# Kernel optimization log

Measured on AMD Instinct MI355X. Metric: run time of the kernel, lower is better.

Reference implementation:

```python
import jax, jax.numpy as jnp
import numpy as np

KQ_DIM = 132  # latent_dim == kq_dim so gather covers full rows
EPS = 1e-12


def setup_inputs() -> dict:
    key = jax.random.key(0)
    ks = jax.random.split(key, 8)
    B, C, H, W = 8, 3, 128, 128
    N, K, D = 2048, 32, KQ_DIM
    indices = jax.random.randint(ks[0], (3, B, N, K), 0, H * W + 1, dtype=jnp.int32)
    img = jax.random.normal(ks[1], (B, C, H, W), dtype=jnp.float32)
    # stand-in backbone: 3x3 conv (ResidualDenseNetwork not in source)
    conv_w = jax.random.normal(ks[2], (D, C, 3, 3), dtype=jnp.float32) * (1.0 / np.sqrt(C * 9))
    conv_b = jnp.zeros((D,), dtype=jnp.float32)
    sc = 1.0 / np.sqrt(D)
    ks_w = jax.random.normal(ks[3], (D, D), dtype=jnp.float32) * sc
    ks_b = jax.random.normal(ks[4], (D,), dtype=jnp.float32) * sc
    qs_w = jax.random.normal(ks[5], (D, D), dtype=jnp.float32) * sc
    qs_b = jax.random.normal(ks[6], (D,), dtype=jnp.float32) * sc
    return {"indices": indices, "img": img, "conv_w": conv_w, "conv_b": conv_b,
            "ks_w": ks_w, "ks_b": ks_b, "qs_w": qs_w, "qs_b": qs_b}


def reference(indices, img, conv_w, conv_b, ks_w, ks_b, qs_w, qs_b):
    _, B, N, K = indices.shape
    # backbone conv: [B, D, H, W]
    feat = jax.lax.conv_general_dilated(
        img, conv_w, window_strides=(1, 1), padding='SAME',
        dimension_numbers=('NCHW', 'OIHW', 'NCHW')) + conv_b[None, :, None, None]
    # torch F.normalize(dim=-1) BEFORE permute -> L2 over last spatial (width) axis
    norm = jnp.linalg.norm(feat, axis=-1, keepdims=True)
    feat = feat / jnp.maximum(norm, EPS)
    # permute(0,2,3,1): [B, H, W, D] -> flatten spatial
    feat = jnp.transpose(feat, (0, 2, 3, 1))
    Bf, Hh, Ww, D = feat.shape
    flat = feat.reshape(Bf, Hh * Ww, D)
    flat = jnp.concatenate([flat, jnp.zeros((Bf, 1, D), dtype=flat.dtype)], axis=1)
    flat_ks = flat @ ks_w.T + ks_b  # [B, WH+1, D]
    flat_qs = flat @ qs_w.T + qs_b
    x_idx = indices[1].reshape(B, N * K)  # [B, N*K]
    y_idx = indices[2].reshape(B, N * K)
    x_feat = jnp.take_along_axis(flat_ks, x_idx[:, :, None], axis=1).reshape(B, N, K, D)
    y_feat = jnp.take_along_axis(flat_qs, y_idx[:, :, None], axis=1).reshape(B, N, K, D)
    # entailment logits: scaled dot product over feature dim
    logits = (x_feat * y_feat).sum(axis=-1) * (D ** -0.5)  # [B, N, K]
    return logits
```

## Files before the change

kernel.cpp:

```cpp
#include <hip/hip_runtime.h>
#include <hip/hip_bf16.h>
#include <math.h>

#define B_ 8
#define H_ 128
#define W_ 128
#define C_ 3
#define D_ 132
#define HW_ (H_*W_)
#define RPB_ (HW_+1)
#define NROWS_ (B_*RPB_)
#define AROWS_ 131136
#define FSTRIDE_ 136
#define MSTRIDE_ 168
#define NK_ 65536
#define NOUT_ (B_*NK_)
#define MELEMS_ 24576

typedef __attribute__((ext_vector_type(8))) short short8v;
typedef __attribute__((ext_vector_type(8))) unsigned short ushort8v;
typedef __attribute__((ext_vector_type(4))) float f32x4;

#define GLOAD16(gp, lp) __builtin_amdgcn_global_load_lds( \
  (const __attribute__((address_space(1))) unsigned int*)(gp), \
  (__attribute__((address_space(3))) unsigned int*)(void*)(lp), 16, 0, 0)

__device__ inline float bf2f(unsigned short u) {
  return __uint_as_float(((unsigned)u) << 16);
}
__device__ inline unsigned short f2bf(float f) {
  __hip_bfloat16 hb = __float2bfloat16(f);
  return *(unsigned short*)&hb;
}

__global__ __launch_bounds__(512, 4) void fused_prep_conv_kernel(
    const float* __restrict__ img, const float* __restrict__ cw,
    const float* __restrict__ cb, unsigned short* __restrict__ flat,
    const float* __restrict__ ks_w, const float* __restrict__ ks_b,
    const float* __restrict__ qs_w, const float* __restrict__ qs_b,
    unsigned short* __restrict__ Mb, float* __restrict__ cc) {
  int bid = blockIdx.x;
  int tid = threadIdx.x;

  if (bid > B_ * H_) {
    int idx = (bid - (B_ * H_ + 1)) * 512 + tid;
    if (idx >= MELEMS_) return;
    int a = idx / MSTRIDE_;
    int k = idx - a * MSTRIDE_;
    float val = 0.f;
    if (k < D_) {
      if (a < D_) {
        for (int o = 0; o < D_; ++o)
          val = fmaf(ks_w[o * D_ + a], qs_w[o * D_ + k], val);
      } else if (a == 132) {
        for (int o = 0; o < D_; ++o)
          val = fmaf(qs_b[o], ks_w[o * D_ + k], val);
      } else if (a == 133) {
        for (int o = 0; o < D_; ++o)
          val = fmaf(ks_b[o], qs_w[o * D_ + k], val);
      }
    }
    Mb[idx] = f2bf(val);
    if (idx == 0) {
      float s = 0.f;
      for (int o = 0; o < D_; ++o) s = fmaf(ks_b[o], qs_b[o], s);
      cc[0] = s;
    }
    return;
  }
  if (bid == B_ * H_) {
    for (int i = tid; i < B_ * FSTRIDE_; i += 512) {
      int b = i / FSTRIDE_, d = i - (i / FSTRIDE_) * FSTRIDE_;
      flat[((size_t)b * RPB_ + HW_) * FSTRIDE_ + d] = (d == 132) ? 0x3F80 : 0;
    }
    return;
  }
  int b = bid >> 7, h = bid & 127;

  __shared__ __align__(16) float in_s[9][132];
  __shared__ float w_s[D_ * 27];
  __shared__ float b_s[D_];
  __shared__ float parts[8][132];
  __shared__ float nscale[132];

  for (int i = tid; i < 9 * 132; i += 512) {
    int ck = i / 132, x = i - ck * 132;
    int c = ck / 3, kh = ck - c * 3;
    int hh = h + kh - 1, ww = x - 1;
    float val = 0.f;
    if (x >= 1 && x <= 128 && hh >= 0 && hh < H_)
      val = img[((size_t)(b * C_ + c) * H_ + hh) * W_ + ww];
    in_s[ck][x] = val;
  }
  for (int i = tid; i < D_ * 27; i += 512) w_s[i] = cw[i];
  if (tid < D_) b_s[tid] = cb[tid];
  __syncthreads();

  auto conv16 = [&](int item, float* acc) {
    int wg = item / 132;
    int d = item - wg * 132;
    float wt[27];
#pragma unroll
    for (int j = 0; j < 27; ++j) wt[j] = w_s[d * 27 + j];
    float bias = b_s[d];
#pragma unroll
    for (int i = 0; i < 16; ++i) acc[i] = bias;
    int q = wg * 4;
#pragma unroll
    for (int ck = 0; ck < 9; ++ck) {
      const float4* p4 = (const float4*)&in_s[ck][0];
      float v[20];
#pragma unroll
      for (int j = 0; j < 5; ++j) {
        float4 t4 = p4[q + j];
        v[4 * j + 0] = t4.x; v[4 * j + 1] = t4.y;
        v[4 * j + 2] = t4.z; v[4 * j + 3] = t4.w;
      }
#pragma unroll
      for (int i = 0; i < 16; ++i) {
        float a0 = fmaf(v[i], wt[ck * 3 + 0], acc[i]);
        float a1 = fmaf(v[i + 1], wt[ck * 3 + 1], a0);
        acc[i] = fmaf(v[i + 2], wt[ck * 3 + 2], a1);
      }
    }
    float ssq = 0.f;
#pragma unroll
    for (int i = 0; i < 16; ++i) ssq = fmaf(acc[i], acc[i], ssq);
    parts[wg][d] = ssq;
  };

  float acc0[16], acc1[16], acc2[16];
  conv16(tid, acc0);
  conv16(tid + 512, acc1);
  if (tid < 32) conv16(tid + 1024, acc2);
  __syncthreads();

  if (tid < 132) {
    float s = 0.f;
#pragma unroll
    for (int wg = 0; wg < 8; ++wg) s += parts[wg][tid];
    nscale[tid] = 1.f / fmaxf(sqrtf(s), 1e-12f);
  }
  __syncthreads();

  size_t rowbase = (size_t)b * RPB_ + (size_t)h * W_;
  auto store16 = [&](int item, const float* acc) {
    int wg = item / 132;
    int d = item - wg * 132;
    float sc = nscale[d];
#pragma unroll
    for (int i = 0; i < 16; ++i)
      flat[(rowbase + wg * 16 + i) * FSTRIDE_ + d] = f2bf(acc[i] * sc);
  };
  store16(tid, acc0);
  store16(tid + 512, acc1);
  if (tid < 32) store16(tid + 1024, acc2);

  if (tid < 128) {
    uint2 tailv; tailv.x = 0x3F80u; tailv.y = 0u;
    *(uint2*)&flat[(rowbase + tid) * FSTRIDE_ + 132] = tailv;
  }
}

__global__ __launch_bounds__(256, 2) void gemm_kernel(
    unsigned short* __restrict__ fb, const unsigned short* __restrict__ Mb,
    const float* __restrict__ cc, unsigned short* __restrict__ zb) {
  __shared__ __align__(16) unsigned short As[64 * FSTRIDE_ + 64];
  __shared__ __align__(16) unsigned short Ms[MELEMS_];
  int tid = threadIdx.x, wave = tid >> 6, lane = tid & 63;
  size_t row0 = (size_t)blockIdx.x * 64;

  for (int ch = wave; ch < 48; ch += 4)
    GLOAD16(Mb + (size_t)ch * 512 + lane * 8, Ms + ch * 512);
  const unsigned short* Ag = fb + row0 * FSTRIDE_;
  for (int ch = wave; ch < 17; ch += 4)
    GLOAD16(Ag + (size_t)ch * 512 + lane * 8, As + ch * 512);
  if (tid < 64) As[64 * FSTRIDE_ + tid] = 0;
  __syncthreads();

  int c15 = lane & 15, kg = lane >> 4;
  const unsigned short* arow = &As[(wave * 16 + c15) * FSTRIDE_ + kg * 8];
  const unsigned short* brow = &Ms[c15 * MSTRIDE_ + kg * 8];
  f32x4 acc[9] = {};
#pragma unroll
  for (int ks = 0; ks < 5; ++ks) {
    short8v af = *(const short8v*)(arow + ks * 32);
#pragma unroll
    for (int ct = 0; ct < 9; ++ct) {
      short8v bf = *(const short8v*)(brow + ct * 16 * MSTRIDE_ + ks * 32);
      acc[ct] = __builtin_amdgcn_mfma_f32_16x16x32_bf16(af, bf, acc[ct], 0, 0, 0);
    }
  }

  float cval = cc[0];
  size_t rbase = row0 + wave * 16 + kg * 4;
#pragma unroll
  for (int ct = 0; ct < 9; ++ct) {
    int col = ct * 16 + c15;
#pragma unroll
    for (int j = 0; j < 4; ++j) {
      size_t r = rbase + j;
      if (r < NROWS_) {
        if (col < D_)            zb[r * FSTRIDE_ + col] = f2bf(acc[ct][j]);
        else if (col == 132)     fb[r * FSTRIDE_ + 133] = f2bf(acc[ct][j]);
        else if (col == 133)     zb[r * FSTRIDE_ + 132] = f2bf(acc[ct][j] + cval);
        else if (col == 134)     zb[r * FSTRIDE_ + 133] = 0x3F80;
        else if (col == 135)     zb[r * FSTRIDE_ + 134] = 0;
        else if (col == 136)     zb[r * FSTRIDE_ + 135] = 0;
      }
    }
  }
}

__global__ __launch_bounds__(256) void gather_kernel(
    const int* __restrict__ xi, const int* __restrict__ yi,
    const unsigned short* __restrict__ flat, const unsigned short* __restrict__ zb,
    float* __restrict__ out) {
  const float scale = 0.08703882797784892f;
  int bi = blockIdx.x;
  int b = bi & 7;
  int chunk = bi >> 3;
  int rem = chunk * 32 + (threadIdx.x >> 3);
  int lane = threadIdx.x & 7;
  size_t ib = (size_t)b * NK_ + rem;
  int x = xi[ib], y = yi[ib];
  const unsigned short* fx = flat + ((size_t)b * RPB_ + x) * FSTRIDE_;
  const unsigned short* zy = zb + ((size_t)b * RPB_ + y) * FSTRIDE_;
  float acc = 0.f;
#pragma unroll
  for (int leg = 0; leg < 2; ++leg) {
    int e0 = leg * 64 + lane * 8;
    ushort8v a8 = *(const ushort8v*)(fx + e0);
    ushort8v z8 = *(const ushort8v*)(zy + e0);
#pragma unroll
    for (int t = 0; t < 8; ++t)
      acc = fmaf(bf2f(a8[t]), bf2f(z8[t]), acc);
  }
  if (lane == 0) {
    ushort8v a8 = *(const ushort8v*)(fx + 128);
    ushort8v z8 = *(const ushort8v*)(zy + 128);
#pragma unroll
    for (int t = 0; t < 8; ++t)
      acc = fmaf(bf2f(a8[t]), bf2f(z8[t]), acc);
  }
  acc += __shfl_xor(acc, 1);
  acc += __shfl_xor(acc, 2);
  acc += __shfl_xor(acc, 4);
  if (lane == 0)
    out[((size_t)b << 16) | rem] = acc * scale;
}

extern "C" void kernel_launch(void* const* d_in, const int* in_sizes, int n_in,
                              void* d_out, int out_size, void* d_ws, size_t ws_size,
                              hipStream_t stream) {
  const int* indices  = (const int*)d_in[0];
  const float* img    = (const float*)d_in[1];
  const float* conv_w = (const float*)d_in[2];
  const float* conv_b = (const float*)d_in[3];
  const float* ks_w   = (const float*)d_in[4];
  const float* ks_b   = (const float*)d_in[5];
  const float* qs_w   = (const float*)d_in[6];
  const float* qs_b   = (const float*)d_in[7];
  float* out = (float*)d_out;

  char* w = (char*)d_ws;
  unsigned short* flatb = (unsigned short*)w;
  size_t off = (size_t)AROWS_ * FSTRIDE_ * 2;
  unsigned short* zbuf = (unsigned short*)(w + off); off += (size_t)AROWS_ * FSTRIDE_ * 2;
  unsigned short* Mb = (unsigned short*)(w + off);   off += MELEMS_ * 2;
  float* cc = (float*)(w + off);

  const int* xi = indices + (size_t)B_ * NK_;
  const int* yi = indices + (size_t)2 * B_ * NK_;

  hipLaunchKernelGGL(fused_prep_conv_kernel, dim3(B_ * H_ + 1 + MELEMS_ / 512),
                     dim3(512), 0, stream,
                     img, conv_w, conv_b, flatb, ks_w, ks_b, qs_w, qs_b, Mb, cc);
  hipLaunchKernelGGL(gemm_kernel, dim3(AROWS_ / 64), dim3(256), 0, stream,
                     flatb, Mb, cc, zbuf);
  hipLaunchKernelGGL(gather_kernel, dim3(NOUT_ / 32), dim3(256), 0, stream,
                     xi, yi, flatb, zbuf, out);
}
```

Before: 92.35 us.

## Fuse conv/normalize with bilinear GEMM per image row; split weight prep kernel

```diff
diff --git a/kernel.cpp b/kernel.cpp
--- a/kernel.cpp
+++ b/kernel.cpp
@@ -12,10 +12,11 @@
 #define NROWS_ (B_*RPB_)
 #define AROWS_ 131136
 #define FSTRIDE_ 136
-#define MSTRIDE_ 168
+#define MSTRIDE_ 160
+#define MROWS_ 144
+#define MELEMS_ (MROWS_*MSTRIDE_)
 #define NK_ 65536
 #define NOUT_ (B_*NK_)
-#define MELEMS_ 24576
 
 typedef __attribute__((ext_vector_type(8))) short short8v;
 typedef __attribute__((ext_vector_type(8))) unsigned short ushort8v;
@@ -33,56 +34,102 @@
   return *(unsigned short*)&hb;
 }
 
-__global__ __launch_bounds__(512, 4) void fused_prep_conv_kernel(
-    const float* __restrict__ img, const float* __restrict__ cw,
-    const float* __restrict__ cb, unsigned short* __restrict__ flat,
+__global__ __launch_bounds__(512) void prep_kernel(
     const float* __restrict__ ks_w, const float* __restrict__ ks_b,
     const float* __restrict__ qs_w, const float* __restrict__ qs_b,
     unsigned short* __restrict__ Mb, float* __restrict__ cc) {
+  int idx = blockIdx.x * 512 + threadIdx.x;
+  if (idx >= MELEMS_) return;
+  int a = idx / MSTRIDE_;
+  int k = idx - a * MSTRIDE_;
+  float val = 0.f;
+  if (k < D_) {
+    if (a < D_) {
+      for (int o = 0; o < D_; ++o)
+        val = fmaf(ks_w[o * D_ + a], qs_w[o * D_ + k], val);
+    } else if (a == 132) {
+      for (int o = 0; o < D_; ++o)
+        val = fmaf(qs_b[o], ks_w[o * D_ + k], val);
+    } else if (a == 133) {
+      for (int o = 0; o < D_; ++o)
+        val = fmaf(ks_b[o], qs_w[o * D_ + k], val);
+    }
+  }
+  Mb[idx] = f2bf(val);
+  if (idx == 0) {
+    float s = 0.f;
+    for (int o = 0; o < D_; ++o) s = fmaf(ks_b[o], qs_b[o], s);
+    cc[0] = s;
+  }
+}
+
+__device__ __forceinline__ float conv_item16(
+    const float* __restrict__ in_s, const float* __restrict__ w_s,
+    float bias, int d, int w0, float* acc) {
+  float wt[27];
+#pragma unroll
+  for (int j = 0; j < 27; ++j) wt[j] = w_s[d * 27 + j];
+#pragma unroll
+  for (int i = 0; i < 16; ++i) acc[i] = bias;
+#pragma unroll
+  for (int ck = 0; ck < 9; ++ck) {
+    const float4* p4 = (const float4*)(in_s + ck * 132);
+    float v[20];
+#pragma unroll
+    for (int j = 0; j < 5; ++j) {
+      float4 t4 = p4[(w0 >> 2) + j];
+      v[4 * j + 0] = t4.x; v[4 * j + 1] = t4.y;
+      v[4 * j + 2] = t4.z; v[4 * j + 3] = t4.w;
+    }
+#pragma unroll
+    for (int i = 0; i < 16; ++i) {
+      float a0 = fmaf(v[i], wt[ck * 3 + 0], acc[i]);
+      float a1 = fmaf(v[i + 1], wt[ck * 3 + 1], a0);
+      acc[i] = fmaf(v[i + 2], wt[ck * 3 + 2], a1);
+    }
+  }
+  float ssq = 0.f;
+#pragma unroll
+  for (int i = 0; i < 16; ++i) ssq = fmaf(acc[i], acc[i], ssq);
+  return ssq;
+}
+
+__global__ __launch_bounds__(512, 4) void fused_conv_gemm_kernel(
+    const float* __restrict__ img, const float* __restrict__ cw,
+    const float* __restrict__ cb, unsigned short* __restrict__ fb,
+    const unsigned short* __restrict__ Mb, const float* __restrict__ cc,
+    unsigned short* __restrict__ zb) {
   int bid = blockIdx.x;
   int tid = threadIdx.x;
 
-  if (bid > B_ * H_) {
-    int idx = (bid - (B_ * H_ + 1)) * 512 + tid;
-    if (idx >= MELEMS_) return;
-    int a = idx / MSTRIDE_;
-    int k = idx - a * MSTRIDE_;
-    float val = 0.f;
-    if (k < D_) {
-      if (a < D_) {
-        for (int o = 0; o < D_; ++o)
-          val = fmaf(ks_w[o * D_ + a], qs_w[o * D_ + k], val);
-      } else if (a == 132) {
-        for (int o = 0; o < D_; ++o)
-          val = fmaf(qs_b[o], ks_w[o * D_ + k], val);
-      } else if (a == 133) {
-        for (int o = 0; o < D_; ++o)
-          val = fmaf(ks_b[o], qs_w[o * D_ + k], val);
-      }
-    }
-    Mb[idx] = f2bf(val);
-    if (idx == 0) {
-      float s = 0.f;
-      for (int o = 0; o < D_; ++o) s = fmaf(ks_b[o], qs_b[o], s);
-      cc[0] = s;
-    }
-    return;
-  }
   if (bid == B_ * H_) {
+    float cval = cc[0];
     for (int i = tid; i < B_ * FSTRIDE_; i += 512) {
       int b = i / FSTRIDE_, d = i - (i / FSTRIDE_) * FSTRIDE_;
-      flat[((size_t)b * RPB_ + HW_) * FSTRIDE_ + d] = (d == 132) ? 0x3F80 : 0;
+      size_t r = (size_t)b * RPB_ + HW_;
+      fb[r * FSTRIDE_ + d] = (d == 132) ? 0x3F80 : 0;
+      unsigned short zv = 0;
+      if (d == 132) zv = f2bf(cval);
+      else if (d == 133) zv = 0x3F80;
+      zb[r * FSTRIDE_ + d] = zv;
     }
     return;
   }
+
+  int wave = tid >> 6, lane = tid & 63;
+  __shared__ __align__(16) unsigned short Ms[MELEMS_];
+  __shared__ float nscale[132];
+  __shared__ __align__(16) char un[34880];
+  float* in_s = (float*)un;
+  float* w_s  = in_s + 9 * 132;
+  float* b_s  = w_s + 132 * 27;
+  float* parts = b_s + 132;
+  unsigned short* As = (unsigned short*)un;
+
+  for (int ch = wave; ch < 45; ch += 8)
+    GLOAD16(Mb + (size_t)ch * 512 + lane * 8, Ms + ch * 512);
+
   int b = bid >> 7, h = bid & 127;
-
-  __shared__ __align__(16) float in_s[9][132];
-  __shared__ float w_s[D_ * 27];
-  __shared__ float b_s[D_];
-  __shared__ float parts[8][132];
-  __shared__ float nscale[132];
-
   for (int i = tid; i < 9 * 132; i += 512) {
     int ck = i / 132, x = i - ck * 132;
     int c = ck / 3, kh = ck - c * 3;
@@ -90,97 +137,64 @@
     float val = 0.f;
     if (x >= 1 && x <= 128 && hh >= 0 && hh < H_)
       val = img[((size_t)(b * C_ + c) * H_ + hh) * W_ + ww];
-    in_s[ck][x] = val;
+    in_s[i] = val;
   }
   for (int i = tid; i < D_ * 27; i += 512) w_s[i] = cw[i];
   if (tid < D_) b_s[tid] = cb[tid];
   __syncthreads();
 
-  auto conv16 = [&](int item, float* acc) {
-    int wg = item / 132;
-    int d = item - wg * 132;
-    float wt[27];
-#pragma unroll
-    for (int j = 0; j < 27; ++j) wt[j] = w_s[d * 27 + j];
-    float bias = b_s[d];
-#pragma unroll
-    for (int i = 0; i < 16; ++i) acc[i] = bias;
-    int q = wg * 4;
-#pragma unroll
-    for (int ck = 0; ck < 9; ++ck) {
-      const float4* p4 = (const float4*)&in_s[ck][0];
-      float v[20];
-#pragma unroll
-      for (int j = 0; j < 5; ++j) {
-        float4 t4 = p4[q + j];
-        v[4 * j + 0] = t4.x; v[4 * j + 1] = t4.y;
-        v[4 * j + 2] = t4.z; v[4 * j + 3] = t4.w;
-      }
-#pragma unroll
-      for (int i = 0; i < 16; ++i) {
-        float a0 = fmaf(v[i], wt[ck * 3 + 0], acc[i]);
-        float a1 = fmaf(v[i + 1], wt[ck * 3 + 1], a0);
-        acc[i] = fmaf(v[i + 2], wt[ck * 3 + 2], a1);
-      }
-    }
-    float ssq = 0.f;
-#pragma unroll
-    for (int i = 0; i < 16; ++i) ssq = fmaf(acc[i], acc[i], ssq);
-    parts[wg][d] = ssq;
-  };
-
   float acc0[16], acc1[16], acc2[16];
-  conv16(tid, acc0);
-  conv16(tid + 512, acc1);
-  if (tid < 32) conv16(tid + 1024, acc2);
-  __syncthreads();
-
+  int i0 = tid, i1 = tid + 512;
+  int wg0 = i0 / 132, dd0 = i0 - wg0 * 132;
+  int wg1 = i1 / 132, dd1 = i1 - wg1 * 132;
+  parts[wg0 * 132 + dd0] = conv_item16(in_s, w_s, b_s[dd0], dd0, wg0 * 16, acc0);
+  parts[wg1 * 132 + dd1] = conv_item16(in_s, w_s, b_s[dd1], dd1, wg1 * 16, acc1);
+  int dd2 = 0;
+  if (tid < 32) {
+    dd2 = 100 + tid;
+    parts[7 * 132 + dd2] = conv_item16(in_s, w_s, b_s[dd2], dd2, 112, acc2);
+  }
+  __syncthreads();
   if (tid < 132) {
     float s = 0.f;
 #pragma unroll
-    for (int wg = 0; wg < 8; ++wg) s += parts[wg][tid];
+    for (int rr = 0; rr < 8; ++rr) s += parts[rr * 132 + tid];
     nscale[tid] = 1.f / fmaxf(sqrtf(s), 1e-12f);
   }
   __syncthreads();
 
   size_t rowbase = (size_t)b * RPB_ + (size_t)h * W_;
-  auto store16 = [&](int item, const float* acc) {
-    int wg = item / 132;
-    int d = item - wg * 132;
-    float sc = nscale[d];
+  {
+    float sc = nscale[dd0];
 #pragma unroll
     for (int i = 0; i < 16; ++i)
-      flat[(rowbase + wg * 16 + i) * FSTRIDE_ + d] = f2bf(acc[i] * sc);
-  };
-  store16(tid, acc0);
-  store16(tid + 512, acc1);
-  if (tid < 32) store16(tid + 1024, acc2);
-
+      fb[(rowbase + wg0 * 16 + i) * FSTRIDE_ + dd0] = f2bf(acc0[i] * sc);
+    sc = nscale[dd1];
+#pragma unroll
+    for (int i = 0; i < 16; ++i)
+      fb[(rowbase + wg1 * 16 + i) * FSTRIDE_ + dd1] = f2bf(acc1[i] * sc);
+  }
+  if (tid < 32) {
+    float sc = nscale[dd2];
+#pragma unroll
+    for (int i = 0; i < 16; ++i)
+      fb[(rowbase + 112 + i) * FSTRIDE_ + dd2] = f2bf(acc2[i] * sc);
+  }
   if (tid < 128) {
-    uint2 tailv; tailv.x = 0x3F80u; tailv.y = 0u;
-    *(uint2*)&flat[(rowbase + tid) * FSTRIDE_ + 132] = tailv;
-  }
-}
-
-__global__ __launch_bounds__(256, 2) void gemm_kernel(
-    unsigned short* __restrict__ fb, const unsigned short* __restrict__ Mb,
-    const float* __restrict__ cc, unsigned short* __restrict__ zb) {
-  __shared__ __align__(16) unsigned short As[64 * FSTRIDE_ + 64];
-  __shared__ __align__(16) unsigned short Ms[MELEMS_];
-  int tid = threadIdx.x, wave = tid >> 6, lane = tid & 63;
-  size_t row0 = (size_t)blockIdx.x * 64;
-
-  for (int ch = wave; ch < 48; ch += 4)
-    GLOAD16(Mb + (size_t)ch * 512 + lane * 8, Ms + ch * 512);
-  const unsigned short* Ag = fb + row0 * FSTRIDE_;
-  for (int ch = wave; ch < 17; ch += 4)
+    uint2 tv; tv.x = 0x3F80u; tv.y = 0u;
+    *(uint2*)&fb[(rowbase + tid) * FSTRIDE_ + 132] = tv;
+  }
+  __syncthreads();
+
+  const unsigned short* Ag = fb + rowbase * FSTRIDE_;
+  for (int ch = wave; ch < 34; ch += 8)
     GLOAD16(Ag + (size_t)ch * 512 + lane * 8, As + ch * 512);
-  if (tid < 64) As[64 * FSTRIDE_ + tid] = 0;
+  if (tid < 32) As[128 * FSTRIDE_ + tid] = 0;
   __syncthreads();
 
   int c15 = lane & 15, kg = lane >> 4;
-  const unsigned short* arow = &As[(wave * 16 + c15) * FSTRIDE_ + kg * 8];
-  const unsigned short* brow = &Ms[c15 * MSTRIDE_ + kg * 8];
+  const unsigned short* arow = As + (wave * 16 + c15) * FSTRIDE_ + kg * 8;
+  const unsigned short* brow = Ms + c15 * MSTRIDE_ + kg * 8;
   f32x4 acc[9] = {};
 #pragma unroll
   for (int ks = 0; ks < 5; ++ks) {
@@ -191,23 +205,20 @@
       acc[ct] = __builtin_amdgcn_mfma_f32_16x16x32_bf16(af, bf, acc[ct], 0, 0, 0);
     }
   }
-
   float cval = cc[0];
-  size_t rbase = row0 + wave * 16 + kg * 4;
+  size_t rbase = rowbase + wave * 16 + kg * 4;
 #pragma unroll
   for (int ct = 0; ct < 9; ++ct) {
     int col = ct * 16 + c15;
 #pragma unroll
     for (int j = 0; j < 4; ++j) {
       size_t r = rbase + j;
-      if (r < NROWS_) {
-        if (col < D_)            zb[r * FSTRIDE_ + col] = f2bf(acc[ct][j]);
-        else if (col == 132)     fb[r * FSTRIDE_ + 133] = f2bf(acc[ct][j]);
-        else if (col == 133)     zb[r * FSTRIDE_ + 132] = f2bf(acc[ct][j] + cval);
-        else if (col == 134)     zb[r * FSTRIDE_ + 133] = 0x3F80;
-        else if (col == 135)     zb[r * FSTRIDE_ + 134] = 0;
-        else if (col == 136)     zb[r * FSTRIDE_ + 135] = 0;
-      }
+      if (col < D_)            zb[r * FSTRIDE_ + col] = f2bf(acc[ct][j]);
+      else if (col == 132)     fb[r * FSTRIDE_ + 133] = f2bf(acc[ct][j]);
+      else if (col == 133)     zb[r * FSTRIDE_ + 132] = f2bf(acc[ct][j] + cval);
+      else if (col == 134)     zb[r * FSTRIDE_ + 133] = 0x3F80;
+      else if (col == 135)     zb[r * FSTRIDE_ + 134] = 0;
+      else if (col == 136)     zb[r * FSTRIDE_ + 135] = 0;
     }
   }
 }
@@ -273,11 +284,10 @@
   const int* xi = indices + (size_t)B_ * NK_;
   const int* yi = indices + (size_t)2 * B_ * NK_;
 
-  hipLaunchKernelGGL(fused_prep_conv_kernel, dim3(B_ * H_ + 1 + MELEMS_ / 512),
-                     dim3(512), 0, stream,
-                     img, conv_w, conv_b, flatb, ks_w, ks_b, qs_w, qs_b, Mb, cc);
-  hipLaunchKernelGGL(gemm_kernel, dim3(AROWS_ / 64), dim3(256), 0, stream,
-                     flatb, Mb, cc, zbuf);
+  hipLaunchKernelGGL(prep_kernel, dim3(MELEMS_ / 512), dim3(512), 0, stream,
+                     ks_w, ks_b, qs_w, qs_b, Mb, cc);
+  hipLaunchKernelGGL(fused_conv_gemm_kernel, dim3(B_ * H_ + 1), dim3(512), 0, stream,
+                     img, conv_w, conv_b, flatb, Mb, cc, zbuf);
   hipLaunchKernelGGL(gather_kernel, dim3(NOUT_ / 32), dim3(256), 0, stream,
                      xi, yi, flatb, zbuf, out);
 }
```

Measured after the change: 90.28 us. 2.2% less time.
